# Kernel optimization log

Hardware: AMD Instinct MI355X
Metric: run time of the kernel (lower is better)

## Reference

```python
import jax, jax.numpy as jnp
from jax import lax
import numpy as np

NEG = -1e9  # mask value for invalid actions


def _masked_cat(logits, va):
    # logits/va: [B, K, H, W]; deterministic 'sampling' = argmax of masked logits
    ml = jnp.where(va, logits, jnp.asarray(NEG, logits.dtype))
    lp = jax.nn.log_softmax(ml, axis=1)
    a = jnp.argmax(ml, axis=1).astype(jnp.int32)          # [B,H,W]
    sel = jnp.take_along_axis(lp, a[:, None], axis=1)[:, 0]
    ent = -jnp.sum(jnp.where(va, jnp.exp(lp) * lp, 0.0), axis=1)
    return sel, a, ent


def _head(x, Wh, bh):
    # 1x1 linear head over channel dim: x [B,C,H,W], Wh [K,C]
    return jnp.einsum('bchw,kc->bkhw', x, Wh) + bh[None, :, None, None]


def _scatter1000(vals, mask, ids):
    # scatter per-position vals into [B,1000] at unit ids; inactive -> dropped
    B = vals.shape[0]
    bb = jnp.broadcast_to(jnp.arange(B)[:, None, None], vals.shape).reshape(-1)
    ii = jnp.where(mask, ids, 1000).reshape(-1)
    return jnp.zeros((B, 1000), vals.dtype).at[bb, ii].set(vals.reshape(-1), mode='drop')


def _forward(gf, mf, ff, uf, Wf, bf, Wc, bc, Wd, bd, Wt, bt,
             Wmd, bmd, Wtd, btd, Wtr, btr, Wta, bta, Wpr, bpr, Wpa, bpa, Wra, bra, Wdr, bdr,
             loc, va_move, va_transfer, va_pickup, va_dig, va_sd, va_rc, va_dn, va_fa):
    B, _, H, W = mf.shape
    # AvgPool2d(3,1,1) with count_include_pad=True == window-sum with zero pad / 9
    pooled = lax.reduce_window(mf, 0.0, lax.add, (1, 1, 3, 3), (1, 1, 1, 1),
                               ((0, 0), (0, 0), (1, 1), (1, 1))) / 9.0
    le = pooled + mf
    # per-channel global min/max normalization to [-1, 1]
    mn = le.min(axis=(0, 2, 3), keepdims=True)
    mx = le.max(axis=(0, 2, 3), keepdims=True)
    le = 2.0 * (le - mn) / (mx - mn) - 1.0
    value_feature = jnp.concatenate([mf, uf], axis=1)  # [B,5,H,W]
    uatva = jnp.stack([va_move.any((1, 2)), va_transfer.any((1, 2, 3)), va_pickup.any((1, 2)),
                       va_dig.any(1), va_sd.any(1), va_rc.any(1), va_dn], axis=1)  # [B,7,H,W]
    unit_mask = uatva.any(1)
    factory_mask = va_fa.any(1)
    unit_ids = loc[:, 1].astype(jnp.int32) + 10
    # critic: 1x1 conv -> scatter into [B,1000]
    critic_map = _head(value_feature, Wc, bc)[:, 0]
    critic_value = _scatter1000(critic_map, unit_mask, unit_ids)
    # direction net: conv3x3 + LeakyReLU on [large_embedding, unit_feature]
    dir_in = jnp.concatenate([le, uf], axis=1)  # [B,5,H,W]
    df = lax.conv_general_dilated(dir_in, Wd, (1, 1), 'SAME',
                                  dimension_numbers=('NCHW', 'OIHW', 'NCHW'))
    df = jax.nn.leaky_relu(df + bd[None, :, None, None])  # [B,4,H,W]
    # factory actor (logp/entropy discarded, as in source)
    _, f_act, _ = _masked_cat(_head(ff, Wf, bf), va_fa)
    factory_act = jnp.where(factory_mask, f_act, 0)
    # unit act type
    t_lp, t, t_en = _masked_cat(_head(value_feature, Wt, bt), uatva)
    # per-type params, computed densely and selected by t (MOVE=0,TRANSFER=1,PICKUP=2,DIG=3,SELF_DESTRUCT=4,RECHARGE=5,DO_NOTHING=6)
    lp_mvd, mv_dir, en_mvd = _masked_cat(_head(df, Wmd, bmd), va_move.any(2))
    lp_trd, tr_dir, en_trd = _masked_cat(_head(df, Wtd, btd), va_transfer.any((2, 3)))
    tv = va_transfer.any(3)  # [B,Dir,Res,H,W]
    tr_res_va = jnp.take_along_axis(tv, tr_dir[:, None, None], axis=1)[:, 0]  # [B,Res,H,W]
    lp_trr, tr_res, en_trr = _masked_cat(_head(df, Wtr, btr), tr_res_va)
    ones_amt = jnp.ones((B, Wta.shape[0], H, W), bool)
    lp_tra, tr_amt, en_tra = _masked_cat(_head(df, Wta, bta), ones_amt)
    lp_pkr, pk_res, en_pkr = _masked_cat(_head(df, Wpr, bpr), va_pickup.any(2))
    lp_pka, pk_amt, en_pka = _masked_cat(_head(df, Wpa, bpa), ones_amt)
    lp_rca, rc_amt, en_rca = _masked_cat(_head(df, Wra, bra), ones_amt)
    lp_dgr, dg_rep, en_dgr = _masked_cat(_head(df, Wdr, bdr), va_dig)
    z = jnp.zeros_like(lp_mvd)
    zi = jnp.zeros_like(t)
    lp_by_t = jnp.stack([lp_mvd, lp_trd + lp_trr + lp_tra, lp_pkr + lp_pka, lp_dgr, z, lp_rca, z])
    en_by_t = jnp.stack([en_mvd, en_trd + en_trr + en_tra, en_pkr + en_pka, en_dgr, z, en_rca, z])
    sel = lambda s: jnp.take_along_axis(s, t[None], axis=0)[0]
    total_lp = t_lp + sel(lp_by_t)
    total_en = t_en + sel(en_by_t)
    logp = _scatter1000(total_lp, unit_mask, unit_ids)
    entropy = _scatter1000(total_en, unit_mask, unit_ids)
    direction = sel(jnp.stack([mv_dir, tr_dir, zi, zi, zi, zi, zi]))
    resource = sel(jnp.stack([zi, tr_res, pk_res, zi, zi, zi, zi]))
    amount = sel(jnp.stack([zi, tr_amt, pk_amt, zi, zi, rc_amt, zi]))
    repeat = sel(jnp.stack([zi, zi, zi, dg_rep, zi, zi, zi]))
    # UnitActChannel order: TYPE, DIRECTION, RESOURCE, AMOUNT, REPEAT, N
    chan = jnp.stack([t, direction, resource, amount, repeat, jnp.ones_like(t)], axis=1).astype(jnp.float32)
    unit_act = jnp.where(unit_mask[:, None], chan, 0.0)
    return logp, critic_value, entropy, factory_act.astype(jnp.float32), unit_act


def setup_inputs() -> dict:
    key = jax.random.key(0)
    ks = jax.random.split(key, 40)
    B, H, W = 32, 96, 96
    D, R, A, K, FA, T = 5, 5, 10, 2, 4, 7
    nrm = lambda i, s: jax.random.normal(ks[i], s, jnp.float32)
    brn = lambda i, s: jax.random.bernoulli(ks[i], 0.5, s)
    return dict(
        global_feature=nrm(0, (B, 4)),
        map_feature=nrm(1, (B, 2, H, W)),
        factory_feature=nrm(2, (B, 6, H, W)),
        unit_feature=nrm(3, (B, 3, H, W)),
        location_feature=jax.random.randint(ks[4], (B, 2, H, W), 0, 900, jnp.int32),
        va_move=brn(5, (B, D, K, H, W)),
        va_transfer=brn(6, (B, D, R, A, H, W)),
        va_pickup=brn(7, (B, R, A, H, W)),
        va_dig=brn(8, (B, K, H, W)),
        va_self_destruct=brn(9, (B, K, H, W)),
        va_recharge=brn(10, (B, K, H, W)),
        va_do_nothing=brn(11, (B, H, W)),
        va_factory_act=brn(12, (B, FA, H, W)),
        Wf=nrm(13, (FA, 6)) * 0.1, bf=nrm(14, (FA,)) * 0.1,
        Wc=nrm(15, (1, 5)) * 0.1, bc=nrm(16, (1,)) * 0.1,
        Wd=nrm(17, (4, 5, 3, 3)) * 0.1, bd=nrm(18, (4,)) * 0.1,
        Wt=nrm(19, (T, 5)) * 0.1, bt=nrm(20, (T,)) * 0.1,
        Wmd=nrm(21, (D, 4)) * 0.1, bmd=nrm(22, (D,)) * 0.1,
        Wtd=nrm(23, (D, 4)) * 0.1, btd=nrm(24, (D,)) * 0.1,
        Wtr=nrm(25, (R, 4)) * 0.1, btr=nrm(26, (R,)) * 0.1,
        Wta=nrm(27, (A, 4)) * 0.1, bta=nrm(28, (A,)) * 0.1,
        Wpr=nrm(29, (R, 4)) * 0.1, bpr=nrm(30, (R,)) * 0.1,
        Wpa=nrm(31, (A, 4)) * 0.1, bpa=nrm(32, (A,)) * 0.1,
        Wra=nrm(33, (A, 4)) * 0.1, bra=nrm(34, (A,)) * 0.1,
        Wdr=nrm(35, (K, 4)) * 0.1, bdr=nrm(36, (K,)) * 0.1,
    )


def reference(global_feature, map_feature, factory_feature, unit_feature, location_feature,
              va_move, va_transfer, va_pickup, va_dig, va_self_destruct, va_recharge,
              va_do_nothing, va_factory_act,
              Wf, bf, Wc, bc, Wd, bd, Wt, bt, Wmd, bmd, Wtd, btd, Wtr, btr, Wta, bta,
              Wpr, bpr, Wpa, bpa, Wra, bra, Wdr, bdr):
    return _forward(global_feature, map_feature, factory_feature, unit_feature,
                    Wf, bf, Wc, bc, Wd, bd, Wt, bt, Wmd, bmd, Wtd, btd, Wtr, btr,
                    Wta, bta, Wpr, bpr, Wpa, bpa, Wra, bra, Wdr, bdr,
                    location_feature, va_move, va_transfer, va_pickup, va_dig,
                    va_self_destruct, va_recharge, va_do_nothing, va_factory_act)
```

## Files before the change

kernel.cpp:

```cpp
#include <hip/hip_runtime.h>
#include <hip/hip_bf16.h>

#define HW 9216
#define NB 32

__device__ inline unsigned fenc(float f){
    unsigned u = __float_as_uint(f);
    return (u & 0x80000000u) ? ~u : (u | 0x80000000u);
}
__device__ inline float fdec(unsigned u){
    return __uint_as_float((u & 0x80000000u) ? (u & 0x7fffffffu) : ~u);
}

__global__ __launch_bounds__(256) void k_le(const float* __restrict__ mf,
                                            float* __restrict__ le,
                                            unsigned* __restrict__ mm ){
    int n = blockIdx.x * 256 + threadIdx.x;
    int p = n % HW;
    int bc = n / HW;
    int c = bc & 1;
    int h = p / 96, w = p % 96;
    const float* plane = mf + (size_t)bc * HW;
    float s = 0.f;
    #pragma unroll
    for(int dy=-1; dy<=1; ++dy){
        int y = h + dy;
        if((unsigned)y < 96u){
            #pragma unroll
            for(int dx=-1; dx<=1; ++dx){
                int x = w + dx;
                if((unsigned)x < 96u) s += plane[y*96 + x];
            }
        }
    }
    float v = s * (1.0f/9.0f) + plane[p];
    le[n] = v;

    float mx = v, mn = v;
    #pragma unroll
    for(int o=32; o; o>>=1){
        mx = fmaxf(mx, __shfl_xor(mx, o));
        mn = fminf(mn, __shfl_xor(mn, o));
    }
    __shared__ float smx[4], smn[4];
    int wv = threadIdx.x >> 6;
    if((threadIdx.x & 63) == 0){ smx[wv] = mx; smn[wv] = mn; }
    __syncthreads();
    if(threadIdx.x == 0){
        for(int i=1;i<4;i++){ mx = fmaxf(mx, smx[i]); mn = fminf(mn, smn[i]); }
        atomicMax(&mm[c],     fenc(mx));
        atomicMin(&mm[2 + c], fenc(mn));
    }
}

__global__ __launch_bounds__(256) void k_dirconv(const float* __restrict__ uf,
                                                 const float* __restrict__ le,
                                                 const unsigned* __restrict__ mm,
                                                 const float* __restrict__ Wdw,
                                                 const float* __restrict__ bdw,
                                                 float* __restrict__ df){
    __shared__ float sW[180];
    __shared__ float sb[4];
    for(int i=threadIdx.x; i<180; i+=256) sW[i] = Wdw[i];
    if(threadIdx.x < 4) sb[threadIdx.x] = bdw[threadIdx.x];
    __syncthreads();

    int n = blockIdx.x * 256 + threadIdx.x;
    int b = n / HW, p = n % HW;
    int h = p / 96, w = p % 96;

    float mx0 = fdec(mm[0]), mx1 = fdec(mm[1]);
    float mn0 = fdec(mm[2]), mn1 = fdec(mm[3]);
    float sc0 = 2.f / (mx0 - mn0), sc1 = 2.f / (mx1 - mn1);
    float of0 = -1.f - mn0 * sc0,  of1 = -1.f - mn1 * sc1;

    float acc0 = sb[0], acc1 = sb[1], acc2 = sb[2], acc3 = sb[3];
    #pragma unroll
    for(int i=0;i<5;i++){
        #pragma unroll
        for(int ky=0; ky<3; ky++){
            int y = h + ky - 1;
            if((unsigned)y >= 96u) continue;
            #pragma unroll
            for(int kx=0; kx<3; kx++){
                int x = w + kx - 1;
                if((unsigned)x >= 96u) continue;
                float v;
                if(i < 2) v = le[((size_t)b*2 + i)*HW + y*96 + x] * (i ? sc1 : sc0) + (i ? of1 : of0);
                else      v = uf[((size_t)b*3 + (i-2))*HW + y*96 + x];
                acc0 += v * sW[((0*5+i)*3+ky)*3+kx];
                acc1 += v * sW[((1*5+i)*3+ky)*3+kx];
                acc2 += v * sW[((2*5+i)*3+ky)*3+kx];
                acc3 += v * sW[((3*5+i)*3+ky)*3+kx];
            }
        }
    }
    size_t ob = ((size_t)b*4)*HW + p;
    df[ob + 0*HW] = acc0 > 0.f ? acc0 : 0.01f*acc0;
    df[ob + 1*HW] = acc1 > 0.f ? acc1 : 0.01f*acc1;
    df[ob + 2*HW] = acc2 > 0.f ? acc2 : 0.01f*acc2;
    df[ob + 3*HW] = acc3 > 0.f ? acc3 : 0.01f*acc3;
}

template<int N>
__device__ inline void mcat(const float* x, unsigned mask, float& lp, int& a, float& en){
    float ml[N];
    #pragma unroll
    for(int i=0;i<N;i++) ml[i] = ((mask >> i) & 1u) ? x[i] : -1e9f;
    float m = ml[0]; int am = 0;
    #pragma unroll
    for(int i=1;i<N;i++) if(ml[i] > m){ m = ml[i]; am = i; }
    float S = 0.f, T = 0.f;
    #pragma unroll
    for(int i=0;i<N;i++){
        float d = ml[i] - m;
        float e = expf(d);
        S += e; T += e * d;
    }
    float lS = logf(S);
    lp = -lS;
    a  = am;
    en = lS - T / S;
}

__global__ __launch_bounds__(256) void k_main(
    const float* __restrict__ mf, const float* __restrict__ uf, const float* __restrict__ ff,
    const int* __restrict__ loc,
    const int* __restrict__ vaM, const int* __restrict__ vaT, const int* __restrict__ vaP,
    const int* __restrict__ vaD, const int* __restrict__ vaS, const int* __restrict__ vaR,
    const int* __restrict__ vaN, const int* __restrict__ vaF,
    const float* Wc, const float* bc, const float* Wf, const float* bf,
    const float* Wt, const float* bt, const float* Wmd, const float* bmd,
    const float* Wtd, const float* btd, const float* Wtr, const float* btr,
    const float* Wta, const float* bta, const float* Wpr, const float* bpr,
    const float* Wpa, const float* bpa, const float* Wra, const float* bra,
    const float* Wdr, const float* bdr,
    const float* __restrict__ df,
    float* __restrict__ crm, float* __restrict__ lpm, float* __restrict__ enm,
    int* __restrict__ idx, float* __restrict__ out)
{
    __shared__ float sw[336];
    {
        int t = threadIdx.x;
        #define CPW(off, src, n) for(int i=t;i<(n);i+=256) sw[(off)+i]=(src)[i];
        CPW(0,Wc,5)    CPW(5,bc,1)    CPW(6,Wf,24)   CPW(30,bf,4)
        CPW(34,Wt,35)  CPW(69,bt,7)   CPW(76,Wmd,20) CPW(96,bmd,5)
        CPW(101,Wtd,20) CPW(121,btd,5) CPW(126,Wtr,20) CPW(146,btr,5)
        CPW(151,Wta,40) CPW(191,bta,10) CPW(201,Wpr,20) CPW(221,bpr,5)
        CPW(226,Wpa,40) CPW(266,bpa,10) CPW(276,Wra,40) CPW(316,bra,10)
        CPW(326,Wdr,8)  CPW(334,bdr,2)
        #undef CPW
    }
    __syncthreads();

    int n = blockIdx.x * 256 + threadIdx.x;
    int b = n / HW, p = n % HW;

    const int* vm = vaM + (size_t)b*10*HW + p;
    unsigned mvm = 0;
    #pragma unroll
    for(int d=0; d<5; d++){
        int a0 = vm[(size_t)(d*2+0)*HW] | vm[(size_t)(d*2+1)*HW];
        mvm |= (unsigned)(a0 != 0) << d;
    }
    const int* vt = vaT + (size_t)b*250*HW + p;
    unsigned tv = 0;
    #pragma unroll
    for(int d=0; d<5; d++){
        #pragma unroll
        for(int r=0; r<5; r++){
            int acc = 0;
            #pragma unroll
            for(int a=0; a<10; a++) acc |= vt[(size_t)((d*5+r)*10 + a)*HW];
            tv |= (unsigned)(acc != 0) << (d*5 + r);
        }
    }
    const int* vp = vaP + (size_t)b*50*HW + p;
    unsigned pkm = 0;
    #pragma unroll
    for(int r=0; r<5; r++){
        int acc = 0;
        #pragma unroll
        for(int a=0; a<10; a++) acc |= vp[(size_t)(r*10 + a)*HW];
        pkm |= (unsigned)(acc != 0) << r;
    }
    const int* vd = vaD + (size_t)b*2*HW + p;
    unsigned digm = (unsigned)(vd[0] != 0) | ((unsigned)(vd[HW] != 0) << 1);
    const int* vs = vaS + (size_t)b*2*HW + p;  int sd_any = vs[0] | vs[HW];
    const int* vr = vaR + (size_t)b*2*HW + p;  int rc_any = vr[0] | vr[HW];
    int dn = vaN[(size_t)b*HW + p];
    const int* vfp = vaF + (size_t)b*4*HW + p;
    unsigned fam = 0;
    #pragma unroll
    for(int j=0; j<4; j++) fam |= (unsigned)(vfp[(size_t)j*HW] != 0) << j;

    unsigned uat = (mvm ? 1u:0u) | ((tv ? 1u:0u)<<1) | ((pkm ? 1u:0u)<<2) | ((digm ? 1u:0u)<<3)
                 | ((sd_any ? 1u:0u)<<4) | ((rc_any ? 1u:0u)<<5) | ((dn ? 1u:0u)<<6);
    bool um = (uat != 0);

    float vf5[5];
    vf5[0] = mf[((size_t)b*2+0)*HW + p];
    vf5[1] = mf[((size_t)b*2+1)*HW + p];
    vf5[2] = uf[((size_t)b*3+0)*HW + p];
    vf5[3] = uf[((size_t)b*3+1)*HW + p];
    vf5[4] = uf[((size_t)b*3+2)*HW + p];
    float d4[4];
    #pragma unroll
    for(int o=0;o<4;o++) d4[o] = df[((size_t)b*4+o)*HW + p];
    float f6[6];
    #pragma unroll
    for(int j=0;j<6;j++) f6[j] = ff[((size_t)b*6+j)*HW + p];

    float critic = sw[5];
    #pragma unroll
    for(int c=0;c<5;c++) critic += sw[c] * vf5[c];

    int fact = 0; float fb = -3e38f;
    #pragma unroll
    for(int j=0;j<4;j++){
        float lg = sw[30+j];
        #pragma unroll
        for(int c=0;c<6;c++) lg += sw[6 + j*6 + c] * f6[c];
        float mlv = ((fam >> j) & 1u) ? lg : -1e9f;
        if(mlv > fb){ fb = mlv; fact = j; }
    }

    float tl[7];
    #pragma unroll
    for(int i=0;i<7;i++){
        float s = sw[69+i];
        #pragma unroll
        for(int c=0;c<5;c++) s += sw[34 + i*5 + c] * vf5[c];
        tl[i] = s;
    }
    float t_lp, t_en; int tt;
    mcat<7>(tl, uat, t_lp, tt, t_en);

    float hl[10];

    #pragma unroll
    for(int i=0;i<5;i++){ float s = sw[96+i];
        #pragma unroll
        for(int c=0;c<4;c++) s += sw[76 + i*4 + c] * d4[c]; hl[i]=s; }
    float lpmv, enmv; int mvdir; mcat<5>(hl, mvm, lpmv, mvdir, enmv);

    #pragma unroll
    for(int i=0;i<5;i++){ float s = sw[121+i];
        #pragma unroll
        for(int c=0;c<4;c++) s += sw[101 + i*4 + c] * d4[c]; hl[i]=s; }
    unsigned trd = 0;
    #pragma unroll
    for(int d=0; d<5; d++) trd |= (unsigned)(((tv >> (5*d)) & 31u) != 0) << d;
    float lptd, entd; int trdir; mcat<5>(hl, trd, lptd, trdir, entd);

    #pragma unroll
    for(int i=0;i<5;i++){ float s = sw[146+i];
        #pragma unroll
        for(int c=0;c<4;c++) s += sw[126 + i*4 + c] * d4[c]; hl[i]=s; }
    float lptr, entr; int trres; mcat<5>(hl, (tv >> (trdir*5)) & 31u, lptr, trres, entr);

    #pragma unroll
    for(int i=0;i<10;i++){ float s = sw[191+i];
        #pragma unroll
        for(int c=0;c<4;c++) s += sw[151 + i*4 + c] * d4[c]; hl[i]=s; }
    float lpta, enta; int tramt; mcat<10>(hl, 0x3FFu, lpta, tramt, enta);

    #pragma unroll
    for(int i=0;i<5;i++){ float s = sw[221+i];
        #pragma unroll
        for(int c=0;c<4;c++) s += sw[201 + i*4 + c] * d4[c]; hl[i]=s; }
    float lppr, enpr; int pkres; mcat<5>(hl, pkm, lppr, pkres, enpr);

    #pragma unroll
    for(int i=0;i<10;i++){ float s = sw[266+i];
        #pragma unroll
        for(int c=0;c<4;c++) s += sw[226 + i*4 + c] * d4[c]; hl[i]=s; }
    float lppa, enpa; int pkamt; mcat<10>(hl, 0x3FFu, lppa, pkamt, enpa);

    #pragma unroll
    for(int i=0;i<10;i++){ float s = sw[316+i];
        #pragma unroll
        for(int c=0;c<4;c++) s += sw[276 + i*4 + c] * d4[c]; hl[i]=s; }
    float lpra, enra; int rcamt; mcat<10>(hl, 0x3FFu, lpra, rcamt, enra);

    #pragma unroll
    for(int i=0;i<2;i++){ float s = sw[334+i];
        #pragma unroll
        for(int c=0;c<4;c++) s += sw[326 + i*4 + c] * d4[c]; hl[i]=s; }
    float lpdg, endg; int dgrep; mcat<2>(hl, digm, lpdg, dgrep, endg);

    float lps = 0.f, ens = 0.f; int dir = 0, res = 0, amt = 0, rep = 0;
    switch(tt){
        case 0: lps = lpmv;               ens = enmv;               dir = mvdir; break;
        case 1: lps = lptd + lptr + lpta; ens = entd + entr + enta; dir = trdir; res = trres; amt = tramt; break;
        case 2: lps = lppr + lppa;        ens = enpr + enpa;        res = pkres; amt = pkamt; break;
        case 3: lps = lpdg;               ens = endg;               rep = dgrep; break;
        case 5: lps = lpra;               ens = enra;               amt = rcamt; break;
        default: break;
    }
    float tot_lp = t_lp + lps;
    float tot_en = t_en + ens;

    size_t q = (size_t)b*HW + p;
    crm[q] = critic;
    lpm[q] = tot_lp;
    enm[q] = tot_en;

    out[96000 + q] = (fam != 0) ? (float)fact : 0.f;
    size_t ub = 390912 + (size_t)b*6*HW + p;
    out[ub + 0*HW] = um ? (float)tt  : 0.f;
    out[ub + 1*HW] = um ? (float)dir : 0.f;
    out[ub + 2*HW] = um ? (float)res : 0.f;
    out[ub + 3*HW] = um ? (float)amt : 0.f;
    out[ub + 4*HW] = um ? (float)rep : 0.f;
    out[ub + 5*HW] = um ? 1.f : 0.f;

    if(um){
        int id = loc[((size_t)b*2 + 1)*HW + p] + 10;
        if((unsigned)id < 1000u) atomicMax(&idx[b*1000 + id], p);
    }
}

__global__ __launch_bounds__(256) void k_gather(const int* __restrict__ idx,
                                                const float* __restrict__ crm,
                                                const float* __restrict__ lpm,
                                                const float* __restrict__ enm,
                                                float* __restrict__ out){
    int j = blockIdx.x * 256 + threadIdx.x;
    if(j >= 32000) return;
    int b = j / 1000;
    int pos = idx[j];
    float lp = 0.f, cv = 0.f, en = 0.f;
    if(pos >= 0){
        size_t q = (size_t)b*HW + pos;
        lp = lpm[q]; cv = crm[q]; en = enm[q];
    }
    out[j]          = lp;
    out[32000 + j]  = cv;
    out[64000 + j]  = en;
}

extern "C" void kernel_launch(void* const* d_in, const int* in_sizes, int n_in,
                              void* d_out, int out_size, void* d_ws, size_t ws_size,
                              hipStream_t stream) {
    const float* mf  = (const float*)d_in[1];
    const float* ffp = (const float*)d_in[2];
    const float* ufp = (const float*)d_in[3];
    const int*   loc = (const int*)d_in[4];
    const int* vaM = (const int*)d_in[5];
    const int* vaT = (const int*)d_in[6];
    const int* vaP = (const int*)d_in[7];
    const int* vaD = (const int*)d_in[8];
    const int* vaS = (const int*)d_in[9];
    const int* vaR = (const int*)d_in[10];
    const int* vaN = (const int*)d_in[11];
    const int* vaF = (const int*)d_in[12];
    const float *Wf=(const float*)d_in[13], *bf=(const float*)d_in[14];
    const float *Wc=(const float*)d_in[15], *bc=(const float*)d_in[16];
    const float *Wdw=(const float*)d_in[17], *bdw=(const float*)d_in[18];
    const float *Wt=(const float*)d_in[19], *bt=(const float*)d_in[20];
    const float *Wmd=(const float*)d_in[21], *bmd=(const float*)d_in[22];
    const float *Wtd=(const float*)d_in[23], *btd=(const float*)d_in[24];
    const float *Wtr=(const float*)d_in[25], *btr=(const float*)d_in[26];
    const float *Wta=(const float*)d_in[27], *bta=(const float*)d_in[28];
    const float *Wpr=(const float*)d_in[29], *bpr=(const float*)d_in[30];
    const float *Wpa=(const float*)d_in[31], *bpa=(const float*)d_in[32];
    const float *Wra=(const float*)d_in[33], *bra=(const float*)d_in[34];
    const float *Wdr=(const float*)d_in[35], *bdr=(const float*)d_in[36];

    char* ws = (char*)d_ws;
    float* le  = (float*)(ws + 0);
    float* df  = (float*)(ws + 2359296);
    float* crm = (float*)(ws + 7077888);
    float* lpm = (float*)(ws + 8257536);
    float* enm = (float*)(ws + 9437184);
    int*   idx = (int*)(ws + 10616832);
    unsigned* mm = (unsigned*)(ws + 10744832);

    hipMemsetAsync(mm, 0x00, 8, stream);
    hipMemsetAsync((char*)mm + 8, 0xFF, 8, stream);
    hipMemsetAsync(idx, 0xFF, 128000, stream);

    k_le<<<dim3(2304), dim3(256), 0, stream>>>(mf, le, mm);
    k_dirconv<<<dim3(1152), dim3(256), 0, stream>>>(ufp, le, mm, Wdw, bdw, df);
    k_main<<<dim3(1152), dim3(256), 0, stream>>>(
        mf, ufp, ffp, loc, vaM, vaT, vaP, vaD, vaS, vaR, vaN, vaF,
        Wc, bc, Wf, bf, Wt, bt, Wmd, bmd, Wtd, btd, Wtr, btr,
        Wta, bta, Wpr, bpr, Wpa, bpa, Wra, bra, Wdr, bdr,
        df, crm, lpm, enm, idx, (float*)d_out);
    k_gather<<<dim3(125), dim3(256), 0, stream>>>(idx, crm, lpm, enm, (float*)d_out);
}
```

Measured before the change: 176.2 us.

## Split valid-action mask reduction into separate vectorized kernel with packed bitmasks

Moves the reduction of all valid-action tensors out of the main head kernel into a new k_masks kernel. Each thread handles four positions using int4 loads and writes two packed 32-bit bitmask words per position. The head kernel then reads only those two words instead of hundreds of scalar int loads. The goal is wider, more efficient loads over the large transfer mask tensor and a lighter head kernel, at the cost of an extra launch and a small intermediate buffer. The new kernel launches only 288 blocks, which may leave the GPU underoccupied.

```diff
diff --git a/kernel.cpp b/kernel.cpp
--- a/kernel.cpp
+++ b/kernel.cpp
@@ -102,8 +102,108 @@
     df[ob + 3*HW] = acc3 > 0.f ? acc3 : 0.01f*acc3;
 }
 
+__global__ __launch_bounds__(256) void k_masks(
+    const int* __restrict__ vaM, const int* __restrict__ vaT, const int* __restrict__ vaP,
+    const int* __restrict__ vaD, const int* __restrict__ vaS, const int* __restrict__ vaR,
+    const int* __restrict__ vaN, const int* __restrict__ vaF,
+    unsigned* __restrict__ tvm, unsigned* __restrict__ pkd)
+{
+    int n4 = blockIdx.x * 256 + threadIdx.x;
+    int b  = n4 / (HW/4);
+    int p0 = (n4 - b*(HW/4)) * 4;
+
+    unsigned tvA[4] = {0,0,0,0};
+    {
+        const int* vtb = vaT + (size_t)b*250*HW + p0;
+        #pragma unroll 5
+        for(int g=0; g<25; g++){
+            int4 acc = *(const int4*)(vtb + (size_t)(g*10)*HW);
+            #pragma unroll
+            for(int a=1; a<10; a++){
+                int4 t = *(const int4*)(vtb + (size_t)(g*10+a)*HW);
+                acc.x|=t.x; acc.y|=t.y; acc.z|=t.z; acc.w|=t.w;
+            }
+            tvA[0] |= (unsigned)(acc.x!=0) << g;
+            tvA[1] |= (unsigned)(acc.y!=0) << g;
+            tvA[2] |= (unsigned)(acc.z!=0) << g;
+            tvA[3] |= (unsigned)(acc.w!=0) << g;
+        }
+    }
+    unsigned pkA[4] = {0,0,0,0};
+    {
+        const int* vmb = vaM + (size_t)b*10*HW + p0;
+        #pragma unroll
+        for(int d=0; d<5; d++){
+            int4 k0 = *(const int4*)(vmb + (size_t)(2*d+0)*HW);
+            int4 k1 = *(const int4*)(vmb + (size_t)(2*d+1)*HW);
+            pkA[0] |= (unsigned)((k0.x|k1.x)!=0) << d;
+            pkA[1] |= (unsigned)((k0.y|k1.y)!=0) << d;
+            pkA[2] |= (unsigned)((k0.z|k1.z)!=0) << d;
+            pkA[3] |= (unsigned)((k0.w|k1.w)!=0) << d;
+        }
+    }
+    {
+        const int* vpb = vaP + (size_t)b*50*HW + p0;
+        #pragma unroll
+        for(int r=0; r<5; r++){
+            int4 acc = *(const int4*)(vpb + (size_t)(r*10)*HW);
+            #pragma unroll
+            for(int a=1; a<10; a++){
+                int4 t = *(const int4*)(vpb + (size_t)(r*10+a)*HW);
+                acc.x|=t.x; acc.y|=t.y; acc.z|=t.z; acc.w|=t.w;
+            }
+            pkA[0] |= (unsigned)(acc.x!=0) << (5+r);
+            pkA[1] |= (unsigned)(acc.y!=0) << (5+r);
+            pkA[2] |= (unsigned)(acc.z!=0) << (5+r);
+            pkA[3] |= (unsigned)(acc.w!=0) << (5+r);
+        }
+    }
+    {
+        const int* vdb = vaD + (size_t)b*2*HW + p0;
+        int4 k0 = *(const int4*)(vdb);
+        int4 k1 = *(const int4*)(vdb + (size_t)HW);
+        pkA[0] |= ((unsigned)(k0.x!=0)<<10) | ((unsigned)(k1.x!=0)<<11);
+        pkA[1] |= ((unsigned)(k0.y!=0)<<10) | ((unsigned)(k1.y!=0)<<11);
+        pkA[2] |= ((unsigned)(k0.z!=0)<<10) | ((unsigned)(k1.z!=0)<<11);
+        pkA[3] |= ((unsigned)(k0.w!=0)<<10) | ((unsigned)(k1.w!=0)<<11);
+    }
+    {
+        const int* vsb = vaS + (size_t)b*2*HW + p0;
+        int4 k0 = *(const int4*)(vsb);
+        int4 k1 = *(const int4*)(vsb + (size_t)HW);
+        pkA[0] |= (unsigned)((k0.x|k1.x)!=0)<<12; pkA[1] |= (unsigned)((k0.y|k1.y)!=0)<<12;
+        pkA[2] |= (unsigned)((k0.z|k1.z)!=0)<<12; pkA[3] |= (unsigned)((k0.w|k1.w)!=0)<<12;
+    }
+    {
+        const int* vrb = vaR + (size_t)b*2*HW + p0;
+        int4 k0 = *(const int4*)(vrb);
+        int4 k1 = *(const int4*)(vrb + (size_t)HW);
+        pkA[0] |= (unsigned)((k0.x|k1.x)!=0)<<13; pkA[1] |= (unsigned)((k0.y|k1.y)!=0)<<13;
+        pkA[2] |= (unsigned)((k0.z|k1.z)!=0)<<13; pkA[3] |= (unsigned)((k0.w|k1.w)!=0)<<13;
+    }
+    {
+        int4 k0 = *(const int4*)(vaN + (size_t)b*HW + p0);
+        pkA[0] |= (unsigned)(k0.x!=0)<<14; pkA[1] |= (unsigned)(k0.y!=0)<<14;
+        pkA[2] |= (unsigned)(k0.z!=0)<<14; pkA[3] |= (unsigned)(k0.w!=0)<<14;
+    }
+    {
+        const int* vfb = vaF + (size_t)b*4*HW + p0;
+        #pragma unroll
+        for(int j=0; j<4; j++){
+            int4 k = *(const int4*)(vfb + (size_t)j*HW);
+            pkA[0] |= (unsigned)(k.x!=0) << (15+j);
+            pkA[1] |= (unsigned)(k.y!=0) << (15+j);
+            pkA[2] |= (unsigned)(k.z!=0) << (15+j);
+            pkA[3] |= (unsigned)(k.w!=0) << (15+j);
+        }
+    }
+    size_t q = (size_t)b*HW + p0;
+    *(uint4*)(tvm + q) = make_uint4(tvA[0], tvA[1], tvA[2], tvA[3]);
+    *(uint4*)(pkd + q) = make_uint4(pkA[0], pkA[1], pkA[2], pkA[3]);
+}
+
 template<int N>
-__device__ inline void mcat(const float* x, unsigned mask, float& lp, int& a, float& en){
+__device__ __forceinline__ void mcat(const float* x, unsigned mask, float& lp, int& a, float& en){
     float ml[N];
     #pragma unroll
     for(int i=0;i<N;i++) ml[i] = ((mask >> i) & 1u) ? x[i] : -1e9f;
@@ -123,12 +223,10 @@
     en = lS - T / S;
 }
 
-__global__ __launch_bounds__(256) void k_main(
+__global__ __launch_bounds__(256) void k_heads(
     const float* __restrict__ mf, const float* __restrict__ uf, const float* __restrict__ ff,
     const int* __restrict__ loc,
-    const int* __restrict__ vaM, const int* __restrict__ vaT, const int* __restrict__ vaP,
-    const int* __restrict__ vaD, const int* __restrict__ vaS, const int* __restrict__ vaR,
-    const int* __restrict__ vaN, const int* __restrict__ vaF,
+    const unsigned* __restrict__ tvm, const unsigned* __restrict__ pkd,
     const float* Wc, const float* bc, const float* Wf, const float* bf,
     const float* Wt, const float* bt, const float* Wmd, const float* bmd,
     const float* Wtd, const float* btd, const float* Wtr, const float* btr,
@@ -155,47 +253,20 @@
 
     int n = blockIdx.x * 256 + threadIdx.x;
     int b = n / HW, p = n % HW;
-
-    const int* vm = vaM + (size_t)b*10*HW + p;
-    unsigned mvm = 0;
-    #pragma unroll
-    for(int d=0; d<5; d++){
-        int a0 = vm[(size_t)(d*2+0)*HW] | vm[(size_t)(d*2+1)*HW];
-        mvm |= (unsigned)(a0 != 0) << d;
-    }
-    const int* vt = vaT + (size_t)b*250*HW + p;
-    unsigned tv = 0;
-    #pragma unroll
-    for(int d=0; d<5; d++){
-        #pragma unroll
-        for(int r=0; r<5; r++){
-            int acc = 0;
-            #pragma unroll
-            for(int a=0; a<10; a++) acc |= vt[(size_t)((d*5+r)*10 + a)*HW];
-            tv |= (unsigned)(acc != 0) << (d*5 + r);
-        }
-    }
-    const int* vp = vaP + (size_t)b*50*HW + p;
-    unsigned pkm = 0;
-    #pragma unroll
-    for(int r=0; r<5; r++){
-        int acc = 0;
-        #pragma unroll
-        for(int a=0; a<10; a++) acc |= vp[(size_t)(r*10 + a)*HW];
-        pkm |= (unsigned)(acc != 0) << r;
-    }
-    const int* vd = vaD + (size_t)b*2*HW + p;
-    unsigned digm = (unsigned)(vd[0] != 0) | ((unsigned)(vd[HW] != 0) << 1);
-    const int* vs = vaS + (size_t)b*2*HW + p;  int sd_any = vs[0] | vs[HW];
-    const int* vr = vaR + (size_t)b*2*HW + p;  int rc_any = vr[0] | vr[HW];
-    int dn = vaN[(size_t)b*HW + p];
-    const int* vfp = vaF + (size_t)b*4*HW + p;
-    unsigned fam = 0;
-    #pragma unroll
-    for(int j=0; j<4; j++) fam |= (unsigned)(vfp[(size_t)j*HW] != 0) << j;
+    size_t q = (size_t)b*HW + p;
+
+    unsigned tv = tvm[q];
+    unsigned pk = pkd[q];
+    unsigned mvm  = pk & 31u;
+    unsigned pkm  = (pk >> 5) & 31u;
+    unsigned digm = (pk >> 10) & 3u;
+    unsigned sd1  = (pk >> 12) & 1u;
+    unsigned rc1  = (pk >> 13) & 1u;
+    unsigned dn1  = (pk >> 14) & 1u;
+    unsigned fam  = (pk >> 15) & 15u;
 
     unsigned uat = (mvm ? 1u:0u) | ((tv ? 1u:0u)<<1) | ((pkm ? 1u:0u)<<2) | ((digm ? 1u:0u)<<3)
-                 | ((sd_any ? 1u:0u)<<4) | ((rc_any ? 1u:0u)<<5) | ((dn ? 1u:0u)<<6);
+                 | (sd1<<4) | (rc1<<5) | (dn1<<6);
     bool um = (uat != 0);
 
     float vf5[5];
@@ -301,7 +372,6 @@
     float tot_lp = t_lp + lps;
     float tot_en = t_en + ens;
 
-    size_t q = (size_t)b*HW + p;
     crm[q] = critic;
     lpm[q] = tot_lp;
     enm[q] = tot_en;
@@ -376,15 +446,18 @@
     float* enm = (float*)(ws + 9437184);
     int*   idx = (int*)(ws + 10616832);
     unsigned* mm = (unsigned*)(ws + 10744832);
+    unsigned* tvm = (unsigned*)(ws + 10744848);
+    unsigned* pkd = (unsigned*)(ws + 11924496);
 
     hipMemsetAsync(mm, 0x00, 8, stream);
     hipMemsetAsync((char*)mm + 8, 0xFF, 8, stream);
     hipMemsetAsync(idx, 0xFF, 128000, stream);
 
+    k_masks<<<dim3(288), dim3(256), 0, stream>>>(vaM, vaT, vaP, vaD, vaS, vaR, vaN, vaF, tvm, pkd);
     k_le<<<dim3(2304), dim3(256), 0, stream>>>(mf, le, mm);
     k_dirconv<<<dim3(1152), dim3(256), 0, stream>>>(ufp, le, mm, Wdw, bdw, df);
-    k_main<<<dim3(1152), dim3(256), 0, stream>>>(
-        mf, ufp, ffp, loc, vaM, vaT, vaP, vaD, vaS, vaR, vaN, vaF,
+    k_heads<<<dim3(1152), dim3(256), 0, stream>>>(
+        mf, ufp, ffp, loc, tvm, pkd,
         Wc, bc, Wf, bf, Wt, bt, Wmd, bmd, Wtd, btd, Wtr, btr,
         Wta, bta, Wpr, bpr, Wpa, bpa, Wra, bra, Wdr, bdr,
         df, crm, lpm, enm, idx, (float*)d_out);
```

New measurement: 210.8 us. 1.2x slower.

## Pack valid-action masks into bitfields in a streaming pre-pass before heads

Applied to the files above, without the earlier changes.

Adds a k_bits kernel that streams all int32 valid-action tensors with wide contiguous int4 loads and packs them into 16-bit bitmasks. A second kernel, k_masks2, reduces those bits into per-position transfer and packed mask words. The main kernel is renamed k_heads and now reads two words per position instead of roughly 300 strided int loads. This is meant to replace strided, poorly vectorised mask reads with coalesced bandwidth-bound streaming, at the cost of two extra launches and an intermediate buffer.

```diff
diff --git a/kernel.cpp b/kernel.cpp
--- a/kernel.cpp
+++ b/kernel.cpp
@@ -3,6 +3,7 @@
 
 #define HW 9216
 #define NB 32
+#define NPOS (NB*HW)
 
 __device__ inline unsigned fenc(float f){
     unsigned u = __float_as_uint(f);
@@ -102,8 +103,101 @@
     df[ob + 3*HW] = acc3 > 0.f ? acc3 : 0.01f*acc3;
 }
 
+#define NCHUNK 23112
+__global__ __launch_bounds__(256) void k_bits(
+    const int* __restrict__ vaT, const int* __restrict__ vaM, const int* __restrict__ vaP,
+    const int* __restrict__ vaD, const int* __restrict__ vaS, const int* __restrict__ vaR,
+    const int* __restrict__ vaN, const int* __restrict__ vaF,
+    unsigned short* __restrict__ bits)
+{
+    for(int chunk = blockIdx.x; chunk < NCHUNK; chunk += gridDim.x){
+        const int* src; size_t u16;
+        if(chunk < 18000){      src = vaT + (size_t)chunk*4096;        u16 = (size_t)chunk*256; }
+        else if(chunk < 18720){ int c = chunk-18000; src = vaM + (size_t)c*4096; u16 = 4608000 + (size_t)c*256; }
+        else if(chunk < 22320){ int c = chunk-18720; src = vaP + (size_t)c*4096; u16 = 4792320 + (size_t)c*256; }
+        else if(chunk < 22464){ int c = chunk-22320; src = vaD + (size_t)c*4096; u16 = 5713920 + (size_t)c*256; }
+        else if(chunk < 22608){ int c = chunk-22464; src = vaS + (size_t)c*4096; u16 = 5750784 + (size_t)c*256; }
+        else if(chunk < 22752){ int c = chunk-22608; src = vaR + (size_t)c*4096; u16 = 5787648 + (size_t)c*256; }
+        else if(chunk < 22824){ int c = chunk-22752; src = vaN + (size_t)c*4096; u16 = 5824512 + (size_t)c*256; }
+        else                  { int c = chunk-22824; src = vaF + (size_t)c*4096; u16 = 5842944 + (size_t)c*256; }
+
+        const int4* s4 = (const int4*)src + (size_t)threadIdx.x*4;
+        int4 v0 = s4[0], v1 = s4[1], v2 = s4[2], v3 = s4[3];
+        unsigned m =
+            ((unsigned)(v0.x!=0)    ) | ((unsigned)(v0.y!=0)<<1 ) | ((unsigned)(v0.z!=0)<<2 ) | ((unsigned)(v0.w!=0)<<3 ) |
+            ((unsigned)(v1.x!=0)<<4 ) | ((unsigned)(v1.y!=0)<<5 ) | ((unsigned)(v1.z!=0)<<6 ) | ((unsigned)(v1.w!=0)<<7 ) |
+            ((unsigned)(v2.x!=0)<<8 ) | ((unsigned)(v2.y!=0)<<9 ) | ((unsigned)(v2.z!=0)<<10) | ((unsigned)(v2.w!=0)<<11) |
+            ((unsigned)(v3.x!=0)<<12) | ((unsigned)(v3.y!=0)<<13) | ((unsigned)(v3.z!=0)<<14) | ((unsigned)(v3.w!=0)<<15);
+        bits[u16 + threadIdx.x] = (unsigned short)m;
+    }
+}
+
+__global__ __launch_bounds__(256) void k_masks2(const unsigned char* __restrict__ B,
+                                                unsigned* __restrict__ tvm,
+                                                unsigned* __restrict__ pkd)
+{
+    int t = blockIdx.x * 256 + threadIdx.x;
+    int b  = t / (HW/8);
+    int p8 = t - b*(HW/8);
+
+    unsigned tvw[8] = {0,0,0,0,0,0,0,0};
+    #pragma unroll 5
+    for(int g=0; g<25; g++){
+        unsigned acc = 0;
+        #pragma unroll
+        for(int a=0; a<10; a++)
+            acc |= B[0 + ((size_t)b*250 + g*10 + a)*1152 + p8];
+        #pragma unroll
+        for(int j=0;j<8;j++) tvw[j] |= ((acc>>j)&1u) << g;
+    }
+
+    unsigned pkw[8] = {0,0,0,0,0,0,0,0};
+    #pragma unroll
+    for(int d=0; d<5; d++){
+        unsigned acc = B[9216000 + ((size_t)b*10 + 2*d  )*1152 + p8]
+                     | B[9216000 + ((size_t)b*10 + 2*d+1)*1152 + p8];
+        #pragma unroll
+        for(int j=0;j<8;j++) pkw[j] |= ((acc>>j)&1u) << d;
+    }
+    #pragma unroll 5
+    for(int r=0; r<5; r++){
+        unsigned acc = 0;
+        #pragma unroll
+        for(int a=0; a<10; a++)
+            acc |= B[9584640 + ((size_t)b*50 + r*10 + a)*1152 + p8];
+        #pragma unroll
+        for(int j=0;j<8;j++) pkw[j] |= ((acc>>j)&1u) << (5+r);
+    }
+    {
+        unsigned d0 = B[11427840 + ((size_t)b*2+0)*1152 + p8];
+        unsigned d1 = B[11427840 + ((size_t)b*2+1)*1152 + p8];
+        unsigned sd = B[11501568 + ((size_t)b*2+0)*1152 + p8]
+                    | B[11501568 + ((size_t)b*2+1)*1152 + p8];
+        unsigned rc = B[11575296 + ((size_t)b*2+0)*1152 + p8]
+                    | B[11575296 + ((size_t)b*2+1)*1152 + p8];
+        unsigned dn = B[11649024 + (size_t)b*1152 + p8];
+        #pragma unroll
+        for(int j=0;j<8;j++){
+            pkw[j] |= (((d0>>j)&1u)<<10) | (((d1>>j)&1u)<<11)
+                    | (((sd>>j)&1u)<<12) | (((rc>>j)&1u)<<13) | (((dn>>j)&1u)<<14);
+        }
+        #pragma unroll
+        for(int c=0;c<4;c++){
+            unsigned fv = B[11685888 + ((size_t)b*4+c)*1152 + p8];
+            #pragma unroll
+            for(int j=0;j<8;j++) pkw[j] |= ((fv>>j)&1u) << (15+c);
+        }
+    }
+
+    size_t q = (size_t)b*HW + (size_t)p8*8;
+    *(uint4*)(tvm + q)     = make_uint4(tvw[0],tvw[1],tvw[2],tvw[3]);
+    *(uint4*)(tvm + q + 4) = make_uint4(tvw[4],tvw[5],tvw[6],tvw[7]);
+    *(uint4*)(pkd + q)     = make_uint4(pkw[0],pkw[1],pkw[2],pkw[3]);
+    *(uint4*)(pkd + q + 4) = make_uint4(pkw[4],pkw[5],pkw[6],pkw[7]);
+}
+
 template<int N>
-__device__ inline void mcat(const float* x, unsigned mask, float& lp, int& a, float& en){
+__device__ __forceinline__ void mcat(const float* x, unsigned mask, float& lp, int& a, float& en){
     float ml[N];
     #pragma unroll
     for(int i=0;i<N;i++) ml[i] = ((mask >> i) & 1u) ? x[i] : -1e9f;
@@ -123,12 +217,10 @@
     en = lS - T / S;
 }
 
-__global__ __launch_bounds__(256) void k_main(
+__global__ __launch_bounds__(256) void k_heads(
     const float* __restrict__ mf, const float* __restrict__ uf, const float* __restrict__ ff,
     const int* __restrict__ loc,
-    const int* __restrict__ vaM, const int* __restrict__ vaT, const int* __restrict__ vaP,
-    const int* __restrict__ vaD, const int* __restrict__ vaS, const int* __restrict__ vaR,
-    const int* __restrict__ vaN, const int* __restrict__ vaF,
+    const unsigned* __restrict__ tvm, const unsigned* __restrict__ pkd,
     const float* Wc, const float* bc, const float* Wf, const float* bf,
     const float* Wt, const float* bt, const float* Wmd, const float* bmd,
     const float* Wtd, const float* btd, const float* Wtr, const float* btr,
@@ -155,47 +247,20 @@
 
     int n = blockIdx.x * 256 + threadIdx.x;
     int b = n / HW, p = n % HW;
-
-    const int* vm = vaM + (size_t)b*10*HW + p;
-    unsigned mvm = 0;
-    #pragma unroll
-    for(int d=0; d<5; d++){
-        int a0 = vm[(size_t)(d*2+0)*HW] | vm[(size_t)(d*2+1)*HW];
-        mvm |= (unsigned)(a0 != 0) << d;
-    }
-    const int* vt = vaT + (size_t)b*250*HW + p;
-    unsigned tv = 0;
-    #pragma unroll
-    for(int d=0; d<5; d++){
-        #pragma unroll
-        for(int r=0; r<5; r++){
-            int acc = 0;
-            #pragma unroll
-            for(int a=0; a<10; a++) acc |= vt[(size_t)((d*5+r)*10 + a)*HW];
-            tv |= (unsigned)(acc != 0) << (d*5 + r);
-        }
-    }
-    const int* vp = vaP + (size_t)b*50*HW + p;
-    unsigned pkm = 0;
-    #pragma unroll
-    for(int r=0; r<5; r++){
-        int acc = 0;
-        #pragma unroll
-        for(int a=0; a<10; a++) acc |= vp[(size_t)(r*10 + a)*HW];
-        pkm |= (unsigned)(acc != 0) << r;
-    }
-    const int* vd = vaD + (size_t)b*2*HW + p;
-    unsigned digm = (unsigned)(vd[0] != 0) | ((unsigned)(vd[HW] != 0) << 1);
-    const int* vs = vaS + (size_t)b*2*HW + p;  int sd_any = vs[0] | vs[HW];
-    const int* vr = vaR + (size_t)b*2*HW + p;  int rc_any = vr[0] | vr[HW];
-    int dn = vaN[(size_t)b*HW + p];
-    const int* vfp = vaF + (size_t)b*4*HW + p;
-    unsigned fam = 0;
-    #pragma unroll
-    for(int j=0; j<4; j++) fam |= (unsigned)(vfp[(size_t)j*HW] != 0) << j;
+    size_t q = (size_t)b*HW + p;
+
+    unsigned tv = tvm[q];
+    unsigned pk = pkd[q];
+    unsigned mvm  = pk & 31u;
+    unsigned pkm  = (pk >> 5) & 31u;
+    unsigned digm = (pk >> 10) & 3u;
+    unsigned sd1  = (pk >> 12) & 1u;
+    unsigned rc1  = (pk >> 13) & 1u;
+    unsigned dn1  = (pk >> 14) & 1u;
+    unsigned fam  = (pk >> 15) & 15u;
 
     unsigned uat = (mvm ? 1u:0u) | ((tv ? 1u:0u)<<1) | ((pkm ? 1u:0u)<<2) | ((digm ? 1u:0u)<<3)
-                 | ((sd_any ? 1u:0u)<<4) | ((rc_any ? 1u:0u)<<5) | ((dn ? 1u:0u)<<6);
+                 | (sd1<<4) | (rc1<<5) | (dn1<<6);
     bool um = (uat != 0);
 
     float vf5[5];
@@ -301,7 +366,6 @@
     float tot_lp = t_lp + lps;
     float tot_en = t_en + ens;
 
-    size_t q = (size_t)b*HW + p;
     crm[q] = critic;
     lpm[q] = tot_lp;
     enm[q] = tot_en;
@@ -376,15 +440,20 @@
     float* enm = (float*)(ws + 9437184);
     int*   idx = (int*)(ws + 10616832);
     unsigned* mm = (unsigned*)(ws + 10744832);
+    unsigned* tvm = (unsigned*)(ws + 10744848);
+    unsigned* pkd = (unsigned*)(ws + 11924496);
+    unsigned short* bits = (unsigned short*)(ws + 16777216);
 
     hipMemsetAsync(mm, 0x00, 8, stream);
     hipMemsetAsync((char*)mm + 8, 0xFF, 8, stream);
     hipMemsetAsync(idx, 0xFF, 128000, stream);
 
+    k_bits<<<dim3(2304), dim3(256), 0, stream>>>(vaT, vaM, vaP, vaD, vaS, vaR, vaN, vaF, bits);
     k_le<<<dim3(2304), dim3(256), 0, stream>>>(mf, le, mm);
     k_dirconv<<<dim3(1152), dim3(256), 0, stream>>>(ufp, le, mm, Wdw, bdw, df);
-    k_main<<<dim3(1152), dim3(256), 0, stream>>>(
-        mf, ufp, ffp, loc, vaM, vaT, vaP, vaD, vaS, vaR, vaN, vaF,
+    k_masks2<<<dim3(144), dim3(256), 0, stream>>>((const unsigned char*)bits, tvm, pkd);
+    k_heads<<<dim3(1152), dim3(256), 0, stream>>>(
+        mf, ufp, ffp, loc, tvm, pkd,
         Wc, bc, Wf, bf, Wt, bt, Wmd, bmd, Wtd, btd, Wtr, btr,
         Wta, bta, Wpr, bpr, Wpa, bpa, Wra, bra, Wdr, bdr,
         df, crm, lpm, enm, idx, (float*)d_out);
```

Result: slower. 207.2 us (+17.6%).
